# Optimization experiments

Hardware: AMD Instinct MI355X
Metric: run time of the kernel (lower is better)

Reference implementation:

```python
import jax, jax.numpy as jnp
import numpy as np
from jax import lax

IN_DIM = 128
B, H, W = 4, 64, 64


def setup_inputs() -> dict:
    key = jax.random.key(0)
    ks = jax.random.split(key, 11)
    C = IN_DIM
    c8 = C // 8
    s = lambda k, shape, scale: jax.random.normal(k, shape, dtype=jnp.float32) * scale
    return {
        "x": s(ks[0], (B, C, H, W), 1.0),
        "x_forward": s(ks[1], (B, C, H, W), 1.0),
        "x_backward": s(ks[2], (B, C, H, W), 1.0),
        # 1x1 conv weights stored as [out, in]
        "Wq": s(ks[3], (c8, C), C ** -0.5),
        "bq": jnp.zeros((c8,), jnp.float32),
        "Wk": s(ks[4], (c8, C), C ** -0.5),
        "bk": jnp.zeros((c8,), jnp.float32),
        "Wv": s(ks[5], (C, C), C ** -0.5),
        "bv": jnp.zeros((C,), jnp.float32),
        # 3x3 conv weight [out=C, in=2C, kh, kw]
        "Wf": s(ks[6], (C, 2 * C, 3, 3), (2 * C * 9) ** -0.5),
        "bf": jnp.zeros((C,), jnp.float32),
    }


def _conv1x1(x, w, b):
    # x: [B,C,H,W], w: [O,C] -> [B,O,H,W]
    return jnp.einsum("bchw,oc->bohw", x, w) + b[None, :, None, None]


def reference(x, x_forward, x_backward, Wq, bq, Wk, bk, Wv, bv, Wf, bf):
    Bb, C, Hh, Ww = x.shape
    HW = Hh * Ww
    query = _conv1x1(x_forward, Wq, bq).reshape(Bb, -1, HW)   # [B,c8,HW]
    key = _conv1x1(x, Wk, bk).reshape(Bb, -1, HW)             # [B,c8,HW]
    value = _conv1x1(x_backward, Wv, bv).reshape(Bb, C, HW)   # [B,C,HW]

    # att_score[b, k_pos, q_pos] = key[b,:,k_pos] . query[b,:,q_pos]
    att_score = jnp.einsum("bck,bcq->bkq", key, query)        # [B,HW,HW]
    max_value = jnp.max(att_score, axis=-1)                   # [B,HW]
    idx = jnp.argmax(att_score, axis=-1)                      # [B,HW] int

    selected_value = jnp.take_along_axis(value, idx[:, None, :], axis=2)
    selected_value = selected_value.reshape(Bb, C, Hh, Ww)
    max_value = max_value.reshape(Bb, 1, Hh, Ww)

    front_res = jnp.concatenate([x, selected_value], axis=1)  # [B,2C,H,W]
    front_res = lax.conv_general_dilated(
        front_res, Wf, window_strides=(1, 1), padding="SAME",
        dimension_numbers=("NCHW", "OIHW", "NCHW"),
    ) + bf[None, :, None, None]
    front_res = front_res * max_value
    return x + front_res
```

## Files before the change

### kernel.cpp

```cpp
#include <hip/hip_runtime.h>

#define HW 4096
#define CC 128
#define MARGIN 2e-3f

typedef unsigned short ushort_t;
typedef unsigned int uint_t;
typedef __attribute__((ext_vector_type(8))) short short8;
typedef __attribute__((ext_vector_type(4))) float f32x4;

__device__ __forceinline__ float dot4(float4 a, float4 b) {
    return (a.x*b.x + a.y*b.y) + (a.z*b.z + a.w*b.w);
}

__device__ __forceinline__ ushort_t f2bf(float f) {
    union { float f; uint_t u; } cv; cv.f = f;
    uint_t r = cv.u + 0x7fffu + ((cv.u >> 16) & 1u);
    return (ushort_t)(r >> 16);
}

__device__ __forceinline__ float bf2f(ushort_t h) {
    union { uint_t u; float f; } cv; cv.u = ((uint_t)h) << 16;
    return cv.f;
}

__device__ __forceinline__ void store16(ushort_t* dst, const ushort_t* s) {
    union { ushort_t s[8]; uint4 v; } a, b;
    #pragma unroll
    for (int j = 0; j < 8; j++) { a.s[j] = s[j]; b.s[j] = s[8+j]; }
    *(uint4*)dst = a.v;
    *(uint4*)(dst + 8) = b.v;
}

__device__ __forceinline__ void gl2lds16(const ushort_t* g, ushort_t* l) {
    __builtin_amdgcn_global_load_lds(
        (const __attribute__((address_space(1))) unsigned int*)g,
        (__attribute__((address_space(3))) unsigned int*)l, 16, 0, 0);
}

__global__ __launch_bounds__(256) void prep_kernel(
    const float* __restrict__ x, const float* __restrict__ xf, const float* __restrict__ xb,
    const float* __restrict__ Wq, const float* __restrict__ bq,
    const float* __restrict__ Wk, const float* __restrict__ bk,
    const float* __restrict__ Wv, const float* __restrict__ bv,
    const float* __restrict__ Wf,
    float* __restrict__ Qt, float* __restrict__ Kt, float* __restrict__ V,
    ushort_t* __restrict__ Qs, ushort_t* __restrict__ KB,
    ushort_t* __restrict__ xsel, ushort_t* __restrict__ Wt)
{
    __shared__ __align__(16) unsigned char smem[16704];
    int bid = blockIdx.x;
    int tid = threadIdx.x;

    if (bid < 512) {
        bool isQ = bid < 256;
        int sub = bid & 255;
        int b = sub >> 6, pt = sub & 63;
        const float* src  = isQ ? xf : x;
        const float* W    = isQ ? Wq : Wk;
        const float* bias = isQ ? bq : bk;
        int ph = tid >> 6, pl = tid & 63;
        int p = pt*64 + pl;
        int pg = (b << 12) + p;
        const float* sp = src + ((size_t)b << 19) + p + ((size_t)(ph*32) << 12);

        float acc[16];
        #pragma unroll
        for (int o = 0; o < 16; o++) acc[o] = ph ? 0.f : bias[o];

        for (int cc = 0; cc < 32; cc += 4) {
            float x0 = sp[(size_t)(cc+0) << 12];
            float x1 = sp[(size_t)(cc+1) << 12];
            float x2 = sp[(size_t)(cc+2) << 12];
            float x3 = sp[(size_t)(cc+3) << 12];
            #pragma unroll
            for (int o = 0; o < 16; o++) {
                float4 w = *(const float4*)&W[o*128 + ph*32 + cc];
                acc[o] += w.x*x0 + w.y*x1 + w.z*x2 + w.w*x3;
            }
        }

        float* sAcc = (float*)smem;
        if (ph) {
            float* dst = sAcc + (ph-1)*1088 + pl*17;
            #pragma unroll
            for (int o = 0; o < 16; o++) dst[o] = acc[o];
        }
        __syncthreads();
        if (!ph) {
            const float* s0 = sAcc + pl*17;
            const float* s1 = sAcc + 1088 + pl*17;
            const float* s2 = sAcc + 2176 + pl*17;
            #pragma unroll
            for (int o = 0; o < 16; o++) acc[o] += s0[o] + s1[o] + s2[o];

            float* dstF = isQ ? Qt : Kt;
            float4* df = (float4*)(dstF + (size_t)pg * 16);
            df[0] = make_float4(acc[0],acc[1],acc[2],acc[3]);
            df[1] = make_float4(acc[4],acc[5],acc[6],acc[7]);
            df[2] = make_float4(acc[8],acc[9],acc[10],acc[11]);
            df[3] = make_float4(acc[12],acc[13],acc[14],acc[15]);

            ushort_t h[16], m[16], l[16];
            #pragma unroll
            for (int d = 0; d < 16; d++) {
                h[d] = f2bf(acc[d]);
                float r1 = acc[d] - bf2f(h[d]);
                m[d] = f2bf(r1);
                l[d] = f2bf(r1 - bf2f(m[d]));
            }
            if (isQ) {
                ushort_t* o_ = Qs + (size_t)pg*64;
                store16(o_,      h);
                store16(o_ + 16, m);
                store16(o_ + 32, h);
                store16(o_ + 48, l);
            } else {
                int u = b*256 + (p >> 4);
                int n = p & 15;
                ushort_t* o_ = KB + (size_t)u*1536 + n*32;
                store16(o_,        h); store16(o_ + 16,   h);
                store16(o_ + 512,  m); store16(o_ + 528,  m);
                store16(o_ + 1024, l); store16(o_ + 1040, h);
            }
        }
    } else if (bid < 1536) {
        int vbid = bid - 512;
        int b = vbid >> 8, og = (vbid >> 4) & 15, pt = vbid & 15;
        float* sW = (float*)smem;
        for (int e = tid; e < 1024; e += 256) sW[e] = Wv[og*1024 + e];
        __syncthreads();

        int p = pt*256 + tid;
        const float* sp = xb + ((size_t)b << 19) + p;

        float acc[8];
        #pragma unroll
        for (int j = 0; j < 8; j++) acc[j] = 0.f;

        for (int c4 = 0; c4 < 128; c4 += 4) {
            float x0 = sp[(size_t)(c4+0) << 12];
            float x1 = sp[(size_t)(c4+1) << 12];
            float x2 = sp[(size_t)(c4+2) << 12];
            float x3 = sp[(size_t)(c4+3) << 12];
            #pragma unroll
            for (int j = 0; j < 8; j++) {
                float4 w = *(const float4*)&sW[j*128 + c4];
                acc[j] += w.x*x0 + w.y*x1 + w.z*x2 + w.w*x3;
            }
        }
        float* vr = V + ((size_t)((b << 12) + p))*128 + og*8;
        float4 r0 = make_float4(acc[0]+bv[og*8+0], acc[1]+bv[og*8+1],
                                acc[2]+bv[og*8+2], acc[3]+bv[og*8+3]);
        float4 r1 = make_float4(acc[4]+bv[og*8+4], acc[5]+bv[og*8+5],
                                acc[6]+bv[og*8+6], acc[7]+bv[og*8+7]);
        *(float4*)vr = r0;
        *(float4*)(vr + 4) = r1;
    } else if (bid < 1792) {
        ushort_t* sT = (ushort_t*)smem;
        int xbid = bid - 1536;
        int b = xbid >> 6, y = xbid & 63;
        int cq = tid >> 6, xx = tid & 63;
        const float* src = x + ((size_t)b << 19) + (y << 6) + xx;
        #pragma unroll 4
        for (int k = 0; k < 32; k++) {
            int c = cq*32 + k;
            sT[xx*130 + c] = f2bf(src[(size_t)c << 12]);
        }
        __syncthreads();
        uint_t* dst = (uint_t*)(xsel + ((size_t)(b*4356 + (y+1)*66 + 1))*256);
        #pragma unroll
        for (int k = 0; k < 16; k++) {
            int idx = k*256 + tid;
            int s = idx >> 6, u = idx & 63;
            uint_t v = *(const uint_t*)&sT[s*130 + u*2];
            dst[s*128 + u] = v;
        }
    } else if (bid < 1922) {
        int g = (bid - 1792) * 256 + tid;
        if (g < 33280) {
            int b = g / 8320;
            int rem = g - b * 8320;
            int si = rem >> 5;
            int ch = rem & 31;
            int y, xx;
            if (si < 66)      { y = 0;  xx = si; }
            else if (si < 132){ y = 65; xx = si - 66; }
            else { int t = si - 132; y = 1 + (t >> 1); xx = (t & 1) ? 65 : 0; }
            int site = y * 66 + xx;
            uint4* dst = (uint4*)(xsel + ((size_t)(b*4356 + site))*256);
            dst[ch] = make_uint4(0,0,0,0);
        }
    } else {
        int t = (bid - 1922) * 256 + tid;
        if (t < 36864) {
            int cg = t & 3;
            int o = (t >> 2) & 31;
            int tc = t >> 7;
            int tap = tc % 9;
            int rest = tc / 9;
            int cb = rest & 7, og = rest >> 3;
            union { ushort_t s[8]; uint4 v; } pk;
            #pragma unroll
            for (int j = 0; j < 8; j++) {
                int ci = cg*8 + j;
                pk.s[j] = f2bf(Wf[(size_t)(og*32 + o)*2304 + (cb*32 + ci)*9 + tap]);
            }
            *(uint4*)(Wt + (size_t)t*8) = pk.v;
        }
    }
}

__global__ __launch_bounds__(512, 2) void att_kernel(
    const ushort_t* __restrict__ Qs, const ushort_t* __restrict__ KB,
    float* __restrict__ maxv, int* __restrict__ idxv, int* __restrict__ flags)
{
    __shared__ float sM1[64*33];
    __shared__ int   sI1[64*33];
    __shared__ float sM2[64*33];

    int bid = blockIdx.x;
    int kg = bid & 63, b = bid >> 6;
    int tid = threadIdx.x;
    int wave = tid >> 6, lane = tid & 63;
    int l15 = lane & 15, quad = lane >> 4;

    short8 Bf[4][3];
    const ushort_t* kb = KB + ((size_t)((b*256 + kg*4)*3))*512 + l15*32 + quad*8;
    #pragma unroll
    for (int t = 0; t < 4; t++)
        #pragma unroll
        for (int p = 0; p < 3; p++)
            Bf[t][p] = *(const short8*)(kb + (size_t)(t*3 + p)*512);

    const ushort_t* qbase = Qs + ((size_t)(b*4096 + wave*512 + l15))*64 + quad*8;

    float m1[4], m2[4]; int i1[4];
    #pragma unroll
    for (int t = 0; t < 4; t++) { m1[t] = -1e30f; m2[t] = -1e30f; i1[t] = 0; }

    for (int it = 0; it < 32; it++) {
        const ushort_t* aptr = qbase + it*1024;
        short8 A1 = *(const short8*)aptr;
        short8 A2 = *(const short8*)(aptr + 32);
        f32x4 acc[4];
        #pragma unroll
        for (int t = 0; t < 4; t++) {
            acc[t] = (f32x4)0.f;
            acc[t] = __builtin_amdgcn_mfma_f32_16x16x32_bf16(A1, Bf[t][0], acc[t], 0, 0, 0);
            acc[t] = __builtin_amdgcn_mfma_f32_16x16x32_bf16(A1, Bf[t][1], acc[t], 0, 0, 0);
            acc[t] = __builtin_amdgcn_mfma_f32_16x16x32_bf16(A2, Bf[t][2], acc[t], 0, 0, 0);
        }
        int q0 = wave*512 + it*16 + quad*4;
        #pragma unroll
        for (int r = 0; r < 4; r++) {
            int cand = q0 + r;
            #pragma unroll
            for (int t = 0; t < 4; t++) {
                float d = acc[t][r];
                float old1 = m1[t];
                bool gt = d > old1;
                m1[t] = gt ? d : old1;
                i1[t] = gt ? cand : i1[t];
                m2[t] = __builtin_amdgcn_fmed3f(d, old1, m2[t]);
            }
        }
    }

    #pragma unroll
    for (int t = 0; t < 4; t++) {
        int kl_ = t*16 + l15;
        int slot = wave*4 + quad;
        sM1[kl_*33 + slot] = m1[t];
        sI1[kl_*33 + slot] = i1[t];
        sM2[kl_*33 + slot] = m2[t];
    }
    __syncthreads();
    if (tid < 64) {
        float M1 = -1e30f; int I1 = 0x7fffffff;
        for (int s = 0; s < 32; s++) {
            float m = sM1[tid*33 + s]; int i = sI1[tid*33 + s];
            if (m > M1 || (m == M1 && i < I1)) { M1 = m; I1 = i; }
        }
        float M2 = -1e30f;
        for (int s = 0; s < 32; s++) {
            float m = sM1[tid*33 + s]; int i = sI1[tid*33 + s];
            float cnd = (i == I1) ? sM2[tid*33 + s] : m;
            M2 = fmaxf(M2, cnd);
        }
        int row = (b << 12) + kg*64 + tid;
        maxv[row] = M1; idxv[row] = I1;
        flags[row] = (M1 - M2 < MARGIN) ? 1 : 0;
    }
}

__global__ __launch_bounds__(256) void gather_kernel(
    const float* __restrict__ V, const float* __restrict__ Qt,
    const float* __restrict__ Kt, const int* __restrict__ idxv,
    const int* __restrict__ flags, float* __restrict__ maxv,
    ushort_t* __restrict__ xsel)
{
    __shared__ int sIdx[64];
    __shared__ int sFlag[64];
    __shared__ int sCnt;
    __shared__ float sRm[256];
    __shared__ int   sRi[256];

    int bid = blockIdx.x;
    int b = bid >> 6, pt = bid & 63;
    int tid = threadIdx.x;
    if (tid == 0) sCnt = 0;
    __syncthreads();
    if (tid < 64) {
        int row = (b << 12) + pt*64 + tid;
        sIdx[tid] = idxv[row];
        if (flags[row]) {
            int s = atomicAdd(&sCnt, 1);
            sFlag[s] = tid;
        }
    }
    __syncthreads();

    int n = sCnt;
    for (int e = 0; e < n; e++) {
        int local = sFlag[e];
        int row = (b << 12) + pt*64 + local;
        const float4* Kp = (const float4*)(Kt + (size_t)row*16);
        float4 ka = Kp[0], kbv = Kp[1], kc = Kp[2], kd = Kp[3];
        const float4* Qp = (const float4*)(Qt + ((size_t)b << 12)*16);
        float m = -1e30f; int i = 0;
        #pragma unroll 4
        for (int j = 0; j < 16; j++) {
            int q = tid*16 + j;
            float4 qa = Qp[q*4+0], qb = Qp[q*4+1], qc = Qp[q*4+2], qd = Qp[q*4+3];
            float d = (dot4(ka,qa) + dot4(kbv,qb)) + (dot4(kc,qc) + dot4(kd,qd));
            if (d > m) { m = d; i = q; }
        }
        sRm[tid] = m; sRi[tid] = i;
        __syncthreads();
        #pragma unroll
        for (int s = 128; s > 0; s >>= 1) {
            if (tid < s) {
                float mo = sRm[tid+s]; int io = sRi[tid+s];
                if (mo > sRm[tid] || (mo == sRm[tid] && io < sRi[tid])) {
                    sRm[tid] = mo; sRi[tid] = io;
                }
            }
            __syncthreads();
        }
        if (tid == 0) {
            maxv[row] = sRm[0];
            sIdx[local] = sRi[0];
        }
        __syncthreads();
    }

    int pp = tid >> 2, cq = tid & 3;
    int p = pt*64 + pp;
    int ip = sIdx[pp];
    const float* vrow = V + ((size_t)((b << 12) + ip))*128 + cq*32;
    int site = ((p >> 6) + 1)*66 + (p & 63) + 1;
    ushort_t* dst = xsel + ((size_t)(b*4356 + site))*256 + 128 + cq*32;
    #pragma unroll
    for (int k = 0; k < 4; k++) {
        float4 a = *(const float4*)(vrow + k*8);
        float4 c = *(const float4*)(vrow + k*8 + 4);
        union { ushort_t s[8]; uint4 v; } pk;
        pk.s[0] = f2bf(a.x); pk.s[1] = f2bf(a.y); pk.s[2] = f2bf(a.z); pk.s[3] = f2bf(a.w);
        pk.s[4] = f2bf(c.x); pk.s[5] = f2bf(c.y); pk.s[6] = f2bf(c.z); pk.s[7] = f2bf(c.w);
        *(uint4*)(dst + k*8) = pk.v;
    }
}

__global__ __launch_bounds__(256) void conv_kernel(
    const float* __restrict__ x, const ushort_t* __restrict__ xsel,
    const ushort_t* __restrict__ Wt, const float* __restrict__ bf,
    const float* __restrict__ maxv, float* __restrict__ out)
{
    __shared__ __align__(16) ushort_t sIn[2][336*32];
    __shared__ __align__(16) ushort_t sW[2][9*32*32];

    int bid = blockIdx.x;
    int og = bid & 3, tx = (bid >> 2) & 3, ty = (bid >> 4) & 3, b = bid >> 6;
    int tid = threadIdx.x;
    int wave = tid >> 6, lane = tid & 63;
    int l15 = lane & 15, quad = lane >> 4;

    const ushort_t* xsel_base = xsel + ((size_t)(b*4356 + (ty*16)*66 + tx*16))*256;
    const ushort_t* wt_base   = Wt + (size_t)og*8*9216;

    f32x4 acc[4][2];
    #pragma unroll
    for (int mi = 0; mi < 4; mi++)
        #pragma unroll
        for (int ni = 0; ni < 2; ni++) acc[mi][ni] = (f32x4)0.f;

    int l4q = lane >> 2, l4 = lane & 3;

    for (int r = wave; r < 21; r += 4) {
        int site = r*16 + l4q;
        int iy = site / 18, ix = site - iy*18;
        const ushort_t* g = xsel_base + (size_t)(iy*66 + ix)*256 + l4*8;
        gl2lds16(g, &sIn[0][r*512]);
    }
    for (int r = wave; r < 18; r += 4) {
        const ushort_t* g = wt_base + r*512 + lane*8;
        gl2lds16(g, &sW[0][r*512]);
    }
    __syncthreads();

    for (int cb = 0; cb < 8; cb++) {
        int cur = cb & 1;
        if (cb < 7) {
            int nb = cur ^ 1;
            for (int r = wave; r < 21; r += 4) {
                int site = r*16 + l4q;
                int iy = site / 18, ix = site - iy*18;
                const ushort_t* g = xsel_base + (size_t)(iy*66 + ix)*256 + (cb+1)*32 + l4*8;
                gl2lds16(g, &sIn[nb][r*512]);
            }
            for (int r = wave; r < 18; r += 4) {
                const ushort_t* g = wt_base + (size_t)(cb+1)*9216 + r*512 + lane*8;
                gl2lds16(g, &sW[nb][r*512]);
            }
        }

        #pragma unroll
        for (int tap = 0; tap < 9; tap++) {
            const int dy = tap / 3, dx = tap % 3;
            short8 B0 = *(const short8*)&sW[cur][(tap*32 +      l15)*32 + quad*8];
            short8 B1 = *(const short8*)&sW[cur][(tap*32 + 16 + l15)*32 + quad*8];
            #pragma unroll
            for (int mi = 0; mi < 4; mi++) {
                int row = wave*4 + mi + dy;
                short8 A = *(const short8*)&sIn[cur][(row*18 + l15 + dx)*32 + quad*8];
                acc[mi][0] = __builtin_amdgcn_mfma_f32_16x16x32_bf16(A, B0, acc[mi][0], 0, 0, 0);
                acc[mi][1] = __builtin_amdgcn_mfma_f32_16x16x32_bf16(A, B1, acc[mi][1], 0, 0, 0);
            }
        }
        __syncthreads();
    }

    int y0 = ty*16, x0 = tx*16;
    const float* xb_ = x   + ((size_t)b << 19);
    float*       ob  = out + ((size_t)b << 19);
    const float* mxb = maxv + (b << 12);
    #pragma unroll
    for (int mi = 0; mi < 4; mi++) {
        int y = y0 + wave*4 + mi;
        int p = (y << 6) + x0 + quad*4;
        float4 mv = *(const float4*)&mxb[p];
        #pragma unroll
        for (int ni = 0; ni < 2; ni++) {
            int o = og*32 + ni*16 + l15;
            float bfo = bf[o];
            float4 xv = *(const float4*)&xb_[((size_t)o << 12) + p];
            float4 r;
            r.x = xv.x + mv.x * (acc[mi][ni][0] + bfo);
            r.y = xv.y + mv.y * (acc[mi][ni][1] + bfo);
            r.z = xv.z + mv.z * (acc[mi][ni][2] + bfo);
            r.w = xv.w + mv.w * (acc[mi][ni][3] + bfo);
            *(float4*)&ob[((size_t)o << 12) + p] = r;
        }
    }
}

extern "C" void kernel_launch(void* const* d_in, const int* in_sizes, int n_in,
                              void* d_out, int out_size, void* d_ws, size_t ws_size,
                              hipStream_t stream) {
    (void)in_sizes; (void)n_in; (void)out_size; (void)ws_size;
    const float* x  = (const float*)d_in[0];
    const float* xf = (const float*)d_in[1];
    const float* xb = (const float*)d_in[2];
    const float* Wq = (const float*)d_in[3];
    const float* bq = (const float*)d_in[4];
    const float* Wk = (const float*)d_in[5];
    const float* bk = (const float*)d_in[6];
    const float* Wv = (const float*)d_in[7];
    const float* bv = (const float*)d_in[8];
    const float* Wf = (const float*)d_in[9];
    const float* bf = (const float*)d_in[10];
    float* out = (float*)d_out;

    float* ws   = (float*)d_ws;
    float* Qt   = ws;
    float* Kt   = Qt + 262144;
    float* V    = Kt + 262144;
    float* mx   = V  + 2097152;
    int*   idxv = (int*)(mx + 16384);
    int*   flags= (int*)(idxv + 16384);
    ushort_t* Qs   = (ushort_t*)(flags + 16384);
    ushort_t* KB   = Qs + 1048576;
    ushort_t* xsel = KB + 1572864;
    ushort_t* Wt   = xsel + 4460544;

    hipLaunchKernelGGL(prep_kernel,   dim3(2066), dim3(256), 0, stream,
                       x, xf, xb, Wq, bq, Wk, bk, Wv, bv, Wf,
                       Qt, Kt, V, Qs, KB, xsel, Wt);
    hipLaunchKernelGGL(att_kernel,    dim3(256), dim3(512), 0, stream, Qs, KB, mx, idxv, flags);
    hipLaunchKernelGGL(gather_kernel, dim3(256), dim3(256), 0, stream,
                       V, Qt, Kt, idxv, flags, mx, xsel);
    hipLaunchKernelGGL(conv_kernel,   dim3(256), dim3(256), 0, stream, x, xsel, Wt, bf, mx, out);
}
```

Before: 170.0 us.

## Fuse near-tie refinement into attention and value gather into conv

Removes the separate gather kernel. The exact fp32 refinement of near-tie rows now runs at the end of the attention kernel using 512 threads. The conv kernel gathers the selected value rows directly from V by index, converting them to bf16 into shared memory for the second half of the input channels, so the selected-value half of the padded buffer is no longer written and re-read. This cuts one launch and a global round trip. In exchange the conv pipeline carries extra register-held prefetch and scattered row loads, and the zero-border fill now covers only the x half.

```diff
diff --git a/kernel.cpp b/kernel.cpp
--- a/kernel.cpp
+++ b/kernel.cpp
@@ -176,13 +176,13 @@
             uint_t v = *(const uint_t*)&sT[s*130 + u*2];
             dst[s*128 + u] = v;
         }
-    } else if (bid < 1922) {
+    } else if (bid < 1857) {
         int g = (bid - 1792) * 256 + tid;
-        if (g < 33280) {
-            int b = g / 8320;
-            int rem = g - b * 8320;
-            int si = rem >> 5;
-            int ch = rem & 31;
+        if (g < 16640) {
+            int b = g / 4160;
+            int rem = g - b * 4160;
+            int si = rem >> 4;
+            int ch = rem & 15;
             int y, xx;
             if (si < 66)      { y = 0;  xx = si; }
             else if (si < 132){ y = 65; xx = si - 66; }
@@ -192,7 +192,7 @@
             dst[ch] = make_uint4(0,0,0,0);
         }
     } else {
-        int t = (bid - 1922) * 256 + tid;
+        int t = (bid - 1857) * 256 + tid;
         if (t < 36864) {
             int cg = t & 3;
             int o = (t >> 2) & 31;
@@ -213,11 +213,14 @@
 
 __global__ __launch_bounds__(512, 2) void att_kernel(
     const ushort_t* __restrict__ Qs, const ushort_t* __restrict__ KB,
-    float* __restrict__ maxv, int* __restrict__ idxv, int* __restrict__ flags)
+    const float* __restrict__ Qt, const float* __restrict__ Kt,
+    float* __restrict__ maxv, int* __restrict__ idxv)
 {
     __shared__ float sM1[64*33];
     __shared__ int   sI1[64*33];
     __shared__ float sM2[64*33];
+    __shared__ int sCnt;
+    __shared__ int sList[64];
 
     int bid = blockIdx.x;
     int kg = bid & 63, b = bid >> 6;
@@ -275,6 +278,7 @@
         sI1[kl_*33 + slot] = i1[t];
         sM2[kl_*33 + slot] = m2[t];
     }
+    if (tid == 0) sCnt = 0;
     __syncthreads();
     if (tid < 64) {
         float M1 = -1e30f; int I1 = 0x7fffffff;
@@ -290,56 +294,34 @@
         }
         int row = (b << 12) + kg*64 + tid;
         maxv[row] = M1; idxv[row] = I1;
-        flags[row] = (M1 - M2 < MARGIN) ? 1 : 0;
-    }
-}
-
-__global__ __launch_bounds__(256) void gather_kernel(
-    const float* __restrict__ V, const float* __restrict__ Qt,
-    const float* __restrict__ Kt, const int* __restrict__ idxv,
-    const int* __restrict__ flags, float* __restrict__ maxv,
-    ushort_t* __restrict__ xsel)
-{
-    __shared__ int sIdx[64];
-    __shared__ int sFlag[64];
-    __shared__ int sCnt;
-    __shared__ float sRm[256];
-    __shared__ int   sRi[256];
-
-    int bid = blockIdx.x;
-    int b = bid >> 6, pt = bid & 63;
-    int tid = threadIdx.x;
-    if (tid == 0) sCnt = 0;
+        if (M1 - M2 < MARGIN) {
+            int s = atomicAdd(&sCnt, 1);
+            sList[s] = tid;
+        }
+    }
     __syncthreads();
-    if (tid < 64) {
-        int row = (b << 12) + pt*64 + tid;
-        sIdx[tid] = idxv[row];
-        if (flags[row]) {
-            int s = atomicAdd(&sCnt, 1);
-            sFlag[s] = tid;
-        }
-    }
-    __syncthreads();
 
     int n = sCnt;
+    float* sRm = sM1;
+    int*   sRi = sI1;
     for (int e = 0; e < n; e++) {
-        int local = sFlag[e];
-        int row = (b << 12) + pt*64 + local;
+        int local = sList[e];
+        int row = (b << 12) + kg*64 + local;
         const float4* Kp = (const float4*)(Kt + (size_t)row*16);
-        float4 ka = Kp[0], kbv = Kp[1], kc = Kp[2], kd = Kp[3];
-        const float4* Qp = (const float4*)(Qt + ((size_t)b << 12)*16);
+        float4 ka = Kp[0], kb2 = Kp[1], kc = Kp[2], kd = Kp[3];
+        const float4* Qp = (const float4*)(Qt + (((size_t)b) << 12)*16);
         float m = -1e30f; int i = 0;
-        #pragma unroll 4
-        for (int j = 0; j < 16; j++) {
-            int q = tid*16 + j;
+        #pragma unroll
+        for (int j = 0; j < 8; j++) {
+            int q = tid*8 + j;
             float4 qa = Qp[q*4+0], qb = Qp[q*4+1], qc = Qp[q*4+2], qd = Qp[q*4+3];
-            float d = (dot4(ka,qa) + dot4(kbv,qb)) + (dot4(kc,qc) + dot4(kd,qd));
+            float d = (dot4(ka,qa) + dot4(kb2,qb)) + (dot4(kc,qc) + dot4(kd,qd));
             if (d > m) { m = d; i = q; }
         }
         sRm[tid] = m; sRi[tid] = i;
         __syncthreads();
         #pragma unroll
-        for (int s = 128; s > 0; s >>= 1) {
+        for (int s = 256; s > 0; s >>= 1) {
             if (tid < s) {
                 float mo = sRm[tid+s]; int io = sRi[tid+s];
                 if (mo > sRm[tid] || (mo == sRm[tid] && io < sRi[tid])) {
@@ -348,54 +330,46 @@
             }
             __syncthreads();
         }
-        if (tid == 0) {
-            maxv[row] = sRm[0];
-            sIdx[local] = sRi[0];
-        }
+        if (tid == 0) { maxv[row] = sRm[0]; idxv[row] = sRi[0]; }
         __syncthreads();
-    }
-
-    int pp = tid >> 2, cq = tid & 3;
-    int p = pt*64 + pp;
-    int ip = sIdx[pp];
-    const float* vrow = V + ((size_t)((b << 12) + ip))*128 + cq*32;
-    int site = ((p >> 6) + 1)*66 + (p & 63) + 1;
-    ushort_t* dst = xsel + ((size_t)(b*4356 + site))*256 + 128 + cq*32;
-    #pragma unroll
-    for (int k = 0; k < 4; k++) {
-        float4 a = *(const float4*)(vrow + k*8);
-        float4 c = *(const float4*)(vrow + k*8 + 4);
-        union { ushort_t s[8]; uint4 v; } pk;
-        pk.s[0] = f2bf(a.x); pk.s[1] = f2bf(a.y); pk.s[2] = f2bf(a.z); pk.s[3] = f2bf(a.w);
-        pk.s[4] = f2bf(c.x); pk.s[5] = f2bf(c.y); pk.s[6] = f2bf(c.z); pk.s[7] = f2bf(c.w);
-        *(uint4*)(dst + k*8) = pk.v;
     }
 }
 
 __global__ __launch_bounds__(256) void conv_kernel(
     const float* __restrict__ x, const ushort_t* __restrict__ xsel,
+    const float* __restrict__ V, const int* __restrict__ idxv,
     const ushort_t* __restrict__ Wt, const float* __restrict__ bf,
     const float* __restrict__ maxv, float* __restrict__ out)
 {
     __shared__ __align__(16) ushort_t sIn[2][336*32];
     __shared__ __align__(16) ushort_t sW[2][9*32*32];
+    __shared__ int sIdx[336];
 
     int bid = blockIdx.x;
     int og = bid & 3, tx = (bid >> 2) & 3, ty = (bid >> 4) & 3, b = bid >> 6;
     int tid = threadIdx.x;
     int wave = tid >> 6, lane = tid & 63;
     int l15 = lane & 15, quad = lane >> 4;
+    int l4q = lane >> 2, l4 = lane & 3;
 
     const ushort_t* xsel_base = xsel + ((size_t)(b*4356 + (ty*16)*66 + tx*16))*256;
     const ushort_t* wt_base   = Wt + (size_t)og*8*9216;
+    const float*    vbase     = V + (((size_t)b) << 12)*128;
+
+    for (int e = tid; e < 336; e += 256) {
+        int iy = e / 18, ix = e - iy*18;
+        int gy = ty*16 - 1 + iy, gx = tx*16 - 1 + ix;
+        int v = -1;
+        if ((unsigned)gy < 64u && (unsigned)gx < 64u)
+            v = idxv[(b << 12) + (gy << 6) + gx];
+        sIdx[e] = v;
+    }
 
     f32x4 acc[4][2];
     #pragma unroll
     for (int mi = 0; mi < 4; mi++)
         #pragma unroll
         for (int ni = 0; ni < 2; ni++) acc[mi][ni] = (f32x4)0.f;
-
-    int l4q = lane >> 2, l4 = lane & 3;
 
     for (int r = wave; r < 21; r += 4) {
         int site = r*16 + l4q;
@@ -409,18 +383,39 @@
     }
     __syncthreads();
 
+    float4 rva[6], rvb[6];
+
     for (int cb = 0; cb < 8; cb++) {
-        int cur = cb & 1;
-        if (cb < 7) {
-            int nb = cur ^ 1;
-            for (int r = wave; r < 21; r += 4) {
-                int site = r*16 + l4q;
-                int iy = site / 18, ix = site - iy*18;
-                const ushort_t* g = xsel_base + (size_t)(iy*66 + ix)*256 + (cb+1)*32 + l4*8;
-                gl2lds16(g, &sIn[nb][r*512]);
+        int cur = cb & 1, nb = cur ^ 1;
+        int nxt = cb + 1;
+        bool vpref = false;
+        if (nxt < 8) {
+            if (nxt < 4) {
+                for (int r = wave; r < 21; r += 4) {
+                    int site = r*16 + l4q;
+                    int iy = site / 18, ix = site - iy*18;
+                    const ushort_t* g = xsel_base + (size_t)(iy*66 + ix)*256 + nxt*32 + l4*8;
+                    gl2lds16(g, &sIn[nb][r*512]);
+                }
+            } else {
+                vpref = true;
+                int ch = (nxt - 4)*32 + l4*8;
+                int i = 0;
+                for (int r = wave; r < 21; r += 4, i++) {
+                    int site = r*16 + l4q;
+                    int vi = sIdx[site];
+                    if (vi >= 0) {
+                        const float* vp = vbase + (size_t)vi*128 + ch;
+                        rva[i] = *(const float4*)vp;
+                        rvb[i] = *(const float4*)(vp + 4);
+                    } else {
+                        rva[i] = make_float4(0.f,0.f,0.f,0.f);
+                        rvb[i] = make_float4(0.f,0.f,0.f,0.f);
+                    }
+                }
             }
             for (int r = wave; r < 18; r += 4) {
-                const ushort_t* g = wt_base + (size_t)(cb+1)*9216 + r*512 + lane*8;
+                const ushort_t* g = wt_base + (size_t)nxt*9216 + r*512 + lane*8;
                 gl2lds16(g, &sW[nb][r*512]);
             }
         }
@@ -436,6 +431,18 @@
                 short8 A = *(const short8*)&sIn[cur][(row*18 + l15 + dx)*32 + quad*8];
                 acc[mi][0] = __builtin_amdgcn_mfma_f32_16x16x32_bf16(A, B0, acc[mi][0], 0, 0, 0);
                 acc[mi][1] = __builtin_amdgcn_mfma_f32_16x16x32_bf16(A, B1, acc[mi][1], 0, 0, 0);
+            }
+        }
+
+        if (vpref) {
+            int i = 0;
+            for (int r = wave; r < 21; r += 4, i++) {
+                union { ushort_t s[8]; uint4 u; } pk;
+                pk.s[0] = f2bf(rva[i].x); pk.s[1] = f2bf(rva[i].y);
+                pk.s[2] = f2bf(rva[i].z); pk.s[3] = f2bf(rva[i].w);
+                pk.s[4] = f2bf(rvb[i].x); pk.s[5] = f2bf(rvb[i].y);
+                pk.s[6] = f2bf(rvb[i].z); pk.s[7] = f2bf(rvb[i].w);
+                *(uint4*)&sIn[nb][r*512 + lane*8] = pk.u;
             }
         }
         __syncthreads();
@@ -488,17 +495,16 @@
     float* V    = Kt + 262144;
     float* mx   = V  + 2097152;
     int*   idxv = (int*)(mx + 16384);
-    int*   flags= (int*)(idxv + 16384);
-    ushort_t* Qs   = (ushort_t*)(flags + 16384);
+    ushort_t* Qs   = (ushort_t*)(idxv + 16384);
     ushort_t* KB   = Qs + 1048576;
     ushort_t* xsel = KB + 1572864;
     ushort_t* Wt   = xsel + 4460544;
 
-    hipLaunchKernelGGL(prep_kernel,   dim3(2066), dim3(256), 0, stream,
+    hipLaunchKernelGGL(prep_kernel,   dim3(2001), dim3(256), 0, stream,
                        x, xf, xb, Wq, bq, Wk, bk, Wv, bv, Wf,
                        Qt, Kt, V, Qs, KB, xsel, Wt);
-    hipLaunchKernelGGL(att_kernel,    dim3(256), dim3(512), 0, stream, Qs, KB, mx, idxv, flags);
-    hipLaunchKernelGGL(gather_kernel, dim3(256), dim3(256), 0, stream,
-                       V, Qt, Kt, idxv, flags, mx, xsel);
-    hipLaunchKernelGGL(conv_kernel,   dim3(256), dim3(256), 0, stream, x, xsel, Wt, bf, mx, out);
-}
+    hipLaunchKernelGGL(att_kernel,    dim3(256), dim3(512), 0, stream,
+                       Qs, KB, Qt, Kt, mx, idxv);
+    hipLaunchKernelGGL(conv_kernel,   dim3(256), dim3(256), 0, stream,
+                       x, xsel, V, idxv, Wt, bf, mx, out);
+}
```

Result: slower. 183.0 us (+7.7%).
